# Kernel tuning notes

Measured on AMD Instinct MI355X. Metric: run time of the kernel, lower is better.

## Reference

```python
import jax, jax.numpy as jnp
import numpy as np

N_NODES = 100000
N_EDGES = 3200000
D_IN = 128
D_OUT = 128


def setup_inputs() -> dict:
    key = jax.random.key(0)
    k1, k2, k3, k4, k5, k6 = jax.random.split(key, 6)
    x = jax.random.normal(k1, (N_NODES, D_IN), dtype=jnp.float32)
    edge_val = jax.random.uniform(k2, (N_EDGES,), dtype=jnp.float32)
    weight = jax.random.normal(k3, (D_IN, D_OUT), dtype=jnp.float32) / np.sqrt(D_IN)
    bias = jax.random.normal(k4, (D_OUT,), dtype=jnp.float32) * 0.01
    edge_row = jax.random.randint(k5, (N_EDGES,), 0, N_NODES, dtype=jnp.int64)
    edge_col = jax.random.randint(k6, (N_EDGES,), 0, N_NODES, dtype=jnp.int64)
    return {"x": x, "edge_val": edge_val, "weight": weight, "bias": bias,
            "edge_row": edge_row, "edge_col": edge_col}


def reference(x, edge_val, weight, bias, edge_row, edge_col):
    # support = Linear(x): [N, D_out]
    support = jnp.einsum("ni,io->no", x, weight) + bias
    # output = spmm(adj, support): gather source-node features, weight by
    # edge value, scatter-add into destination rows.
    msgs = edge_val[:, None] * support[edge_col]  # [E, D_out]
    output = jax.ops.segment_sum(msgs, edge_row, num_segments=N_NODES)
    return output
```

## Files before the change

### kernel.cpp

```cpp
#include <hip/hip_runtime.h>

#define N_NODES 100000
#define N_EDGES 3200000
#define D 128

#define MT 64
#define BSPAN 32
#define NB 3125
#define CAP 1280
#define PBLOCKS 256
#define PCHUNK (N_EDGES / PBLOCKS)
#define OVF_CAP 8192

#define SUP_OFF     0ULL
#define RECS_OFF    25600000ULL
#define TAILS_OFF   (RECS_OFF + (size_t)NB * CAP * 8)
#define OVFCNT_OFF  (TAILS_OFF + (size_t)NB * 4)
#define OVF_OFF     ((OVFCNT_OFF + 15) & ~15ULL)
#define WS_NEED     (OVF_OFF + (size_t)OVF_CAP * 12)

typedef short short8 __attribute__((ext_vector_type(8)));
typedef float floatx4 __attribute__((ext_vector_type(4)));
typedef unsigned short ushort8v __attribute__((ext_vector_type(8)));

__device__ inline ushort f2bf(float f) {
  uint u = __float_as_uint(f);
  u += 0x7FFF + ((u >> 16) & 1);
  return (ushort)(u >> 16);
}
__device__ inline float bf_lo(uint b) { return __uint_as_float(b << 16); }
__device__ inline float bf_hi(uint b) { return __uint_as_float(b & 0xFFFF0000u); }

#define LSTR 136

__global__ __launch_bounds__(256) void gcn_gemm_mfma(
    const float* __restrict__ x, const float* __restrict__ W,
    const float* __restrict__ bias, ushort* __restrict__ support, int M) {
  __shared__ ushort WT[D * LSTR];
  __shared__ ushort XT[MT * LSTR];

  const int t = threadIdx.x;
  const int w = t >> 6;
  const int lane = t & 63;
  const int quad = lane >> 4;
  const int l16 = lane & 15;
  const int row0 = blockIdx.x * MT;

  for (int i = t * 4; i < D * D; i += 1024) {
    const int k = i >> 7, n = i & 127;
    const float4 wv = *(const float4*)&W[i];
    WT[(n + 0) * LSTR + k] = f2bf(wv.x);
    WT[(n + 1) * LSTR + k] = f2bf(wv.y);
    WT[(n + 2) * LSTR + k] = f2bf(wv.z);
    WT[(n + 3) * LSTR + k] = f2bf(wv.w);
  }
  for (int i = t * 4; i < MT * D; i += 1024) {
    const int m = i >> 7, k = i & 127;
    const int r = row0 + m;
    float4 xv = make_float4(0.f, 0.f, 0.f, 0.f);
    if (r < M) xv = *(const float4*)&x[(size_t)r * D + k];
    ushort4 pv;
    pv.x = f2bf(xv.x); pv.y = f2bf(xv.y); pv.z = f2bf(xv.z); pv.w = f2bf(xv.w);
    *(ushort4*)&XT[m * LSTR + k] = pv;
  }
  __syncthreads();

  floatx4 acc[8];
#pragma unroll
  for (int nt = 0; nt < 8; nt++) acc[nt] = (floatx4)0.f;

#pragma unroll
  for (int kc = 0; kc < 4; kc++) {
    const short8 a = *(const short8*)&XT[(w * 16 + l16) * LSTR + kc * 32 + quad * 8];
#pragma unroll
    for (int nt = 0; nt < 8; nt++) {
      const short8 b = *(const short8*)&WT[(nt * 16 + l16) * LSTR + kc * 32 + quad * 8];
      acc[nt] = __builtin_amdgcn_mfma_f32_16x16x32_bf16(a, b, acc[nt], 0, 0, 0);
    }
  }

  float bs[8];
#pragma unroll
  for (int nt = 0; nt < 8; nt++) bs[nt] = bias[nt * 16 + l16];

  __syncthreads();
#pragma unroll
  for (int nt = 0; nt < 8; nt++)
#pragma unroll
    for (int r = 0; r < 4; r++)
      XT[(w * 16 + quad * 4 + r) * LSTR + nt * 16 + l16] = f2bf(acc[nt][r] + bs[nt]);
  __syncthreads();

  for (int i = t * 8; i < MT * D; i += 2048) {
    const int m = i >> 7, k = i & 127;
    const int r = row0 + m;
    if (r < M)
      *(ushort8v*)&support[(size_t)r * D + k] = *(const ushort8v*)&XT[m * LSTR + k];
  }
}

__global__ __launch_bounds__(1024) void partition_kernel(
    const int* __restrict__ erow, const int* __restrict__ ecol,
    const float* __restrict__ eval, int* __restrict__ tails,
    int2* __restrict__ recs, int* __restrict__ ovf_cnt,
    int3* __restrict__ ovf) {
  __shared__ int cnt[NB];
  __shared__ int cursor[NB];
  const int t = threadIdx.x;
  for (int i = t; i < NB; i += 1024) cnt[i] = 0;
  __syncthreads();

  const int e0 = blockIdx.x * PCHUNK;
  for (int e = e0 + t; e < e0 + PCHUNK; e += 1024)
    atomicAdd(&cnt[erow[e] >> 5], 1);
  __syncthreads();

  for (int i = t; i < NB; i += 1024) {
    const int c = cnt[i];
    cursor[i] = (c > 0) ? atomicAdd(&tails[i], c) : 0;
  }
  __syncthreads();

  for (int e = e0 + t; e < e0 + PCHUNK; e += 1024) {
    const int row = erow[e];
    const int b = row >> 5;
    const int pos = atomicAdd(&cursor[b], 1);
    const int col = ecol[e];
    const int vb = __float_as_int(eval[e]);
    if (pos < CAP) {
      recs[(size_t)b * CAP + pos] = make_int2(col | ((row & 31) << 20), vb);
    } else {
      const int oi = atomicAdd(ovf_cnt, 1);
      if (oi < OVF_CAP) ovf[oi] = make_int3(row, col, vb);
    }
  }
}

__global__ __launch_bounds__(256, 8) void bucket_gather(
    const ushort* __restrict__ sup, const int* __restrict__ tails,
    const int2* __restrict__ recs, float* __restrict__ out) {
  __shared__ int2 lrec[CAP];
  __shared__ int rcnt[BSPAN];
  __shared__ int rstart[BSPAN];
  __shared__ int rend[BSPAN];
  __shared__ int rpos[BSPAN];

  const int bi = blockIdx.x;
  const int t = threadIdx.x;
  const int n = min(tails[bi], CAP);
  const long long* __restrict__ gb64 =
      (const long long*)(recs + (size_t)bi * CAP);

  if (t < BSPAN) rcnt[t] = 0;
  __syncthreads();

  int2 rcache[5];
  int nr = 0;
  for (int i = t; i < n; i += 256) {
    const long long v = __builtin_nontemporal_load(&gb64[i]);
    rcache[nr++] = make_int2((int)(unsigned long long)v, (int)(v >> 32));
  }

  for (int j = 0; j < nr; j++) atomicAdd(&rcnt[rcache[j].x >> 20], 1);
  __syncthreads();

  if (t < BSPAN) {
    const int c = rcnt[t];
    int v = c;
#pragma unroll
    for (int off = 1; off < BSPAN; off <<= 1) {
      const int u = __shfl_up(v, off);
      if (t >= off) v += u;
    }
    rend[t] = v;
    rstart[t] = v - c;
    rpos[t] = v - c;
  }
  __syncthreads();

  for (int j = 0; j < nr; j++) {
    const int2 rc = rcache[j];
    const int p = atomicAdd(&rpos[rc.x >> 20], 1);
    lrec[p] = make_int2((rc.x & 0xFFFFF) << 8, rc.y);
  }
  __syncthreads();

  const int lane = t & 63;
  const int w = t >> 6;
  const int g = lane >> 4;
  const int gl = lane & 15;
  const char* __restrict__ supb = (const char*)sup;

  for (int j = 0; j < 8; j++) {
    const int rr = w * 8 + j;
    const int s = rstart[rr];
    const int e = rend[rr];
    float4 acc0 = make_float4(0.f, 0.f, 0.f, 0.f);
    float4 acc1 = make_float4(0.f, 0.f, 0.f, 0.f);
    for (int i = s; i < e; i += 16) {
      int coff[4];
      float val[4];
      uint4 b[4];
#pragma unroll
      for (int sl = 0; sl < 4; sl++) {
        const int idx = i + sl * 4 + g;
        const int2 rc = lrec[min(idx, CAP - 1)];
        const bool valid = idx < e;
        coff[sl] = valid ? rc.x : 0;
        val[sl] = valid ? __int_as_float(rc.y) : 0.f;
      }
#pragma unroll
      for (int sl = 0; sl < 4; sl++)
        b[sl] = *(const uint4*)(supb + coff[sl] + gl * 16);
#pragma unroll
      for (int sl = 0; sl < 4; sl++) {
        acc0.x += val[sl] * bf_lo(b[sl].x);
        acc0.y += val[sl] * bf_hi(b[sl].x);
        acc0.z += val[sl] * bf_lo(b[sl].y);
        acc0.w += val[sl] * bf_hi(b[sl].y);
        acc1.x += val[sl] * bf_lo(b[sl].z);
        acc1.y += val[sl] * bf_hi(b[sl].z);
        acc1.z += val[sl] * bf_lo(b[sl].w);
        acc1.w += val[sl] * bf_hi(b[sl].w);
      }
    }
#pragma unroll
    for (int off = 16; off <= 32; off <<= 1) {
      acc0.x += __shfl_xor(acc0.x, off);
      acc0.y += __shfl_xor(acc0.y, off);
      acc0.z += __shfl_xor(acc0.z, off);
      acc0.w += __shfl_xor(acc0.w, off);
      acc1.x += __shfl_xor(acc1.x, off);
      acc1.y += __shfl_xor(acc1.y, off);
      acc1.z += __shfl_xor(acc1.z, off);
      acc1.w += __shfl_xor(acc1.w, off);
    }
    const int row = bi * BSPAN + rr;
    if (g == 0 && row < N_NODES) {
      float* op = &out[(size_t)row * D + gl * 8];
      __builtin_nontemporal_store(acc0.x, op + 0);
      __builtin_nontemporal_store(acc0.y, op + 1);
      __builtin_nontemporal_store(acc0.z, op + 2);
      __builtin_nontemporal_store(acc0.w, op + 3);
      __builtin_nontemporal_store(acc1.x, op + 4);
      __builtin_nontemporal_store(acc1.y, op + 5);
      __builtin_nontemporal_store(acc1.z, op + 6);
      __builtin_nontemporal_store(acc1.w, op + 7);
    }
  }
}

__global__ __launch_bounds__(256) void ovf_apply(
    const int* __restrict__ ovf_cnt, const int3* __restrict__ ovf,
    const ushort* __restrict__ sup, float* __restrict__ out) {
  const int tid = blockIdx.x * 256 + threadIdx.x;
  const int e = tid >> 5;
  const int n = min(*ovf_cnt, OVF_CAP);
  if (e >= n) return;
  const int3 rec = ovf[e];
  const float val = __int_as_float(rec.z);
  const int j = (tid & 31) * 4;
#pragma unroll
  for (int k = 0; k < 4; k++) {
    const float f = __uint_as_float(((uint)sup[(size_t)rec.y * D + j + k]) << 16);
    unsafeAtomicAdd(&out[(size_t)rec.x * D + j + k], val * f);
  }
}

__global__ __launch_bounds__(256) void gcn_spmm_atomic(
    const ushort* __restrict__ sup, const float* __restrict__ edge_val,
    const int* __restrict__ edge_row, const int* __restrict__ edge_col,
    float* __restrict__ out) {
  const long long tid = (long long)blockIdx.x * blockDim.x + threadIdx.x;
  const int e = (int)(tid >> 5);
  if (e >= N_EDGES) return;
  const int j = ((int)tid & 31) * 4;
  const int col = edge_col[e];
  const int row = edge_row[e];
  const float val = edge_val[e];
#pragma unroll
  for (int k = 0; k < 4; k++) {
    const float f = __uint_as_float(((uint)sup[(size_t)col * D + j + k]) << 16);
    unsafeAtomicAdd(&out[(size_t)row * D + j + k], val * f);
  }
}

extern "C" void kernel_launch(void* const* d_in, const int* in_sizes, int n_in,
                              void* d_out, int out_size, void* d_ws,
                              size_t ws_size, hipStream_t stream) {
  const float* x        = (const float*)d_in[0];
  const float* edge_val = (const float*)d_in[1];
  const float* W        = (const float*)d_in[2];
  const float* bias     = (const float*)d_in[3];
  const int*   edge_row = (const int*)d_in[4];
  const int*   edge_col = (const int*)d_in[5];
  float* out = (float*)d_out;

  char* ws = (char*)d_ws;
  ushort* support = (ushort*)(ws + SUP_OFF);

  const int gemm_blocks = (N_NODES + MT - 1) / MT;
  gcn_gemm_mfma<<<gemm_blocks, 256, 0, stream>>>(x, W, bias, support, N_NODES);

  if (ws_size >= WS_NEED) {
    int2* recs   = (int2*)(ws + RECS_OFF);
    int*  tails  = (int*)(ws + TAILS_OFF);
    int*  ovfcnt = (int*)(ws + OVFCNT_OFF);
    int3* ovf    = (int3*)(ws + OVF_OFF);

    hipMemsetAsync(tails, 0, (size_t)NB * 4 + 4, stream);
    partition_kernel<<<PBLOCKS, 1024, 0, stream>>>(edge_row, edge_col, edge_val,
                                                   tails, recs, ovfcnt, ovf);
    bucket_gather<<<NB, 256, 0, stream>>>(support, tails, recs, out);
    ovf_apply<<<OVF_CAP * 32 / 256, 256, 0, stream>>>(ovfcnt, ovf, support, out);
  } else {
    hipMemsetAsync(out, 0, (size_t)out_size * sizeof(float), stream);
    const long long spmm_threads = (long long)N_EDGES * 32;
    gcn_spmm_atomic<<<(int)((spmm_threads + 255) / 256), 256, 0, stream>>>(
        support, edge_val, edge_row, edge_col, out);
  }
}
```

Before: 362.2 us.

## Fuse edge partitioning into GEMM launch and shrink overflow-apply grid

Merges the edge bucketing pass and the bf16 MFMA GEMM into one launch. The first 256 blocks partition edges, reusing the GEMM's shared memory for their counters, and the remaining blocks compute the support rows, so the two independent phases can run concurrently. Partition blocks drop from 1024 to 256 threads each, which makes every block do more serial work. Record writes now use nontemporal stores, and the overflow kernel becomes a grid-stride loop over 128 blocks instead of a fixed large grid.

```diff
diff --git a/kernel.cpp b/kernel.cpp
--- a/kernel.cpp
+++ b/kernel.cpp
@@ -33,18 +33,60 @@
 
 #define LSTR 136
 
-__global__ __launch_bounds__(256) void gcn_gemm_mfma(
+__global__ __launch_bounds__(256) void gemm_partition_fused(
     const float* __restrict__ x, const float* __restrict__ W,
-    const float* __restrict__ bias, ushort* __restrict__ support, int M) {
+    const float* __restrict__ bias, ushort* __restrict__ support, int M,
+    const int* __restrict__ erow, const int* __restrict__ ecol,
+    const float* __restrict__ eval, int* __restrict__ tails,
+    int2* __restrict__ recs, int* __restrict__ ovf_cnt,
+    int3* __restrict__ ovf) {
   __shared__ ushort WT[D * LSTR];
   __shared__ ushort XT[MT * LSTR];
 
   const int t = threadIdx.x;
+
+  if (blockIdx.x < PBLOCKS) {
+    int* cnt = (int*)WT;
+    int* cursor = cnt + NB;
+    for (int i = t; i < NB; i += 256) cnt[i] = 0;
+    __syncthreads();
+
+    const int e0 = blockIdx.x * PCHUNK;
+    for (int e = e0 + t; e < e0 + PCHUNK; e += 256)
+      atomicAdd(&cnt[erow[e] >> 5], 1);
+    __syncthreads();
+
+    for (int i = t; i < NB; i += 256) {
+      const int c = cnt[i];
+      cursor[i] = (c > 0) ? atomicAdd(&tails[i], c) : 0;
+    }
+    __syncthreads();
+
+    for (int e = e0 + t; e < e0 + PCHUNK; e += 256) {
+      const int row = erow[e];
+      const int b = row >> 5;
+      const int pos = atomicAdd(&cursor[b], 1);
+      const int col = ecol[e];
+      const int vb = __float_as_int(eval[e]);
+      if (pos < CAP) {
+        const unsigned long long pk =
+            (unsigned)(col | ((row & 31) << 20)) |
+            ((unsigned long long)(unsigned)vb << 32);
+        __builtin_nontemporal_store(
+            (long long)pk, (long long*)&recs[(size_t)b * CAP + pos]);
+      } else {
+        const int oi = atomicAdd(ovf_cnt, 1);
+        if (oi < OVF_CAP) ovf[oi] = make_int3(row, col, vb);
+      }
+    }
+    return;
+  }
+
   const int w = t >> 6;
   const int lane = t & 63;
   const int quad = lane >> 4;
   const int l16 = lane & 15;
-  const int row0 = blockIdx.x * MT;
+  const int row0 = (blockIdx.x - PBLOCKS) * MT;
 
   for (int i = t * 4; i < D * D; i += 1024) {
     const int k = i >> 7, n = i & 127;
@@ -99,40 +141,69 @@
   }
 }
 
-__global__ __launch_bounds__(1024) void partition_kernel(
-    const int* __restrict__ erow, const int* __restrict__ ecol,
-    const float* __restrict__ eval, int* __restrict__ tails,
-    int2* __restrict__ recs, int* __restrict__ ovf_cnt,
-    int3* __restrict__ ovf) {
-  __shared__ int cnt[NB];
-  __shared__ int cursor[NB];
+__global__ __launch_bounds__(256) void gcn_gemm_mfma(
+    const float* __restrict__ x, const float* __restrict__ W,
+    const float* __restrict__ bias, ushort* __restrict__ support, int M) {
+  __shared__ ushort WT[D * LSTR];
+  __shared__ ushort XT[MT * LSTR];
+
   const int t = threadIdx.x;
-  for (int i = t; i < NB; i += 1024) cnt[i] = 0;
-  __syncthreads();
-
-  const int e0 = blockIdx.x * PCHUNK;
-  for (int e = e0 + t; e < e0 + PCHUNK; e += 1024)
-    atomicAdd(&cnt[erow[e] >> 5], 1);
-  __syncthreads();
-
-  for (int i = t; i < NB; i += 1024) {
-    const int c = cnt[i];
-    cursor[i] = (c > 0) ? atomicAdd(&tails[i], c) : 0;
-  }
-  __syncthreads();
-
-  for (int e = e0 + t; e < e0 + PCHUNK; e += 1024) {
-    const int row = erow[e];
-    const int b = row >> 5;
-    const int pos = atomicAdd(&cursor[b], 1);
-    const int col = ecol[e];
-    const int vb = __float_as_int(eval[e]);
-    if (pos < CAP) {
-      recs[(size_t)b * CAP + pos] = make_int2(col | ((row & 31) << 20), vb);
-    } else {
-      const int oi = atomicAdd(ovf_cnt, 1);
-      if (oi < OVF_CAP) ovf[oi] = make_int3(row, col, vb);
-    }
+  const int w = t >> 6;
+  const int lane = t & 63;
+  const int quad = lane >> 4;
+  const int l16 = lane & 15;
+  const int row0 = blockIdx.x * MT;
+
+  for (int i = t * 4; i < D * D; i += 1024) {
+    const int k = i >> 7, n = i & 127;
+    const float4 wv = *(const float4*)&W[i];
+    WT[(n + 0) * LSTR + k] = f2bf(wv.x);
+    WT[(n + 1) * LSTR + k] = f2bf(wv.y);
+    WT[(n + 2) * LSTR + k] = f2bf(wv.z);
+    WT[(n + 3) * LSTR + k] = f2bf(wv.w);
+  }
+  for (int i = t * 4; i < MT * D; i += 1024) {
+    const int m = i >> 7, k = i & 127;
+    const int r = row0 + m;
+    float4 xv = make_float4(0.f, 0.f, 0.f, 0.f);
+    if (r < M) xv = *(const float4*)&x[(size_t)r * D + k];
+    ushort4 pv;
+    pv.x = f2bf(xv.x); pv.y = f2bf(xv.y); pv.z = f2bf(xv.z); pv.w = f2bf(xv.w);
+    *(ushort4*)&XT[m * LSTR + k] = pv;
+  }
+  __syncthreads();
+
+  floatx4 acc[8];
+#pragma unroll
+  for (int nt = 0; nt < 8; nt++) acc[nt] = (floatx4)0.f;
+
+#pragma unroll
+  for (int kc = 0; kc < 4; kc++) {
+    const short8 a = *(const short8*)&XT[(w * 16 + l16) * LSTR + kc * 32 + quad * 8];
+#pragma unroll
+    for (int nt = 0; nt < 8; nt++) {
+      const short8 b = *(const short8*)&WT[(nt * 16 + l16) * LSTR + kc * 32 + quad * 8];
+      acc[nt] = __builtin_amdgcn_mfma_f32_16x16x32_bf16(a, b, acc[nt], 0, 0, 0);
+    }
+  }
+
+  float bs[8];
+#pragma unroll
+  for (int nt = 0; nt < 8; nt++) bs[nt] = bias[nt * 16 + l16];
+
+  __syncthreads();
+#pragma unroll
+  for (int nt = 0; nt < 8; nt++)
+#pragma unroll
+    for (int r = 0; r < 4; r++)
+      XT[(w * 16 + quad * 4 + r) * LSTR + nt * 16 + l16] = f2bf(acc[nt][r] + bs[nt]);
+  __syncthreads();
+
+  for (int i = t * 8; i < MT * D; i += 2048) {
+    const int m = i >> 7, k = i & 127;
+    const int r = row0 + m;
+    if (r < M)
+      *(ushort8v*)&support[(size_t)r * D + k] = *(const ushort8v*)&XT[m * LSTR + k];
   }
 }
 
@@ -253,17 +324,18 @@
 __global__ __launch_bounds__(256) void ovf_apply(
     const int* __restrict__ ovf_cnt, const int3* __restrict__ ovf,
     const ushort* __restrict__ sup, float* __restrict__ out) {
-  const int tid = blockIdx.x * 256 + threadIdx.x;
-  const int e = tid >> 5;
   const int n = min(*ovf_cnt, OVF_CAP);
-  if (e >= n) return;
-  const int3 rec = ovf[e];
-  const float val = __int_as_float(rec.z);
-  const int j = (tid & 31) * 4;
-#pragma unroll
-  for (int k = 0; k < 4; k++) {
-    const float f = __uint_as_float(((uint)sup[(size_t)rec.y * D + j + k]) << 16);
-    unsafeAtomicAdd(&out[(size_t)rec.x * D + j + k], val * f);
+  for (int tid = blockIdx.x * 256 + threadIdx.x; tid < n * 32;
+       tid += 128 * 256) {
+    const int e = tid >> 5;
+    const int3 rec = ovf[e];
+    const float val = __int_as_float(rec.z);
+    const int j = (tid & 31) * 4;
+#pragma unroll
+    for (int k = 0; k < 4; k++) {
+      const float f = __uint_as_float(((uint)sup[(size_t)rec.y * D + j + k]) << 16);
+      unsafeAtomicAdd(&out[(size_t)rec.x * D + j + k], val * f);
+    }
   }
 }
 
@@ -300,7 +372,6 @@
   ushort* support = (ushort*)(ws + SUP_OFF);
 
   const int gemm_blocks = (N_NODES + MT - 1) / MT;
-  gcn_gemm_mfma<<<gemm_blocks, 256, 0, stream>>>(x, W, bias, support, N_NODES);
 
   if (ws_size >= WS_NEED) {
     int2* recs   = (int2*)(ws + RECS_OFF);
@@ -309,11 +380,13 @@
     int3* ovf    = (int3*)(ws + OVF_OFF);
 
     hipMemsetAsync(tails, 0, (size_t)NB * 4 + 4, stream);
-    partition_kernel<<<PBLOCKS, 1024, 0, stream>>>(edge_row, edge_col, edge_val,
-                                                   tails, recs, ovfcnt, ovf);
+    gemm_partition_fused<<<PBLOCKS + gemm_blocks, 256, 0, stream>>>(
+        x, W, bias, support, N_NODES,
+        edge_row, edge_col, edge_val, tails, recs, ovfcnt, ovf);
     bucket_gather<<<NB, 256, 0, stream>>>(support, tails, recs, out);
-    ovf_apply<<<OVF_CAP * 32 / 256, 256, 0, stream>>>(ovfcnt, ovf, support, out);
+    ovf_apply<<<128, 256, 0, stream>>>(ovfcnt, ovf, support, out);
   } else {
+    gcn_gemm_mfma<<<gemm_blocks, 256, 0, stream>>>(x, W, bias, support, N_NODES);
     hipMemsetAsync(out, 0, (size_t)out_size * sizeof(float), stream);
     const long long spmm_threads = (long long)N_EDGES * 32;
     gcn_spmm_atomic<<<(int)((spmm_threads + 255) / 256), 256, 0, stream>>>(
```

Result: slower. 400.7 us (+10.6%).
